# Optimization experiments

Hardware: AMD Instinct MI355X
Metric: run time of the kernel (lower is better)

Reference implementation:

```python
import jax, jax.numpy as jnp
import numpy as np

LEAK = 0.01
TEMP = 1.0
N_ORB = 1024
CTX = 32
N_ALPHA = 32
N_BETA = 32
B = 8192
EPS = 1e-20


def _leaky(x):
    return jnp.where(x >= 0, x, LEAK * x)


def _scorer_mlp(x, W1, b1, W2, b2, W3, b3):
    h = _leaky(x @ W1 + b1)
    h = _leaky(h @ W2 + b2)
    return h @ W3 + b3


def _gumbel_topk(logits, gumbel, k, temp):
    # successive-softmax subset relaxation (Plackett-Luce style)
    scores0 = logits + gumbel

    def step(carry, _):
        scores, khot = carry
        onehot = jax.nn.softmax(scores / temp, axis=-1)
        khot = khot + onehot
        scores = scores + jnp.log(jnp.maximum(1.0 - onehot, EPS))
        return (scores, khot), None

    (_, khot), _ = jax.lax.scan(step, (scores0, jnp.zeros_like(scores0)), None, length=k)
    return khot


def _soft_to_hard(soft, k):
    # straight-through: hard forward, soft backward
    idx = jax.lax.top_k(soft, k)[1]                      # (B, k)
    bidx = jnp.arange(soft.shape[0])[:, None]
    hard = jnp.zeros_like(soft).at[bidx, idx].set(1.0)
    return jax.lax.stop_gradient(hard - soft) + soft


def _lin_init(key, fan_in, fan_out):
    s = 1.0 / np.sqrt(fan_in)
    k1, k2 = jax.random.split(key)
    W = jax.random.uniform(k1, (fan_in, fan_out), minval=-s, maxval=s, dtype=jnp.float32)
    b = jax.random.uniform(k2, (fan_out,), minval=-s, maxval=s, dtype=jnp.float32)
    return W, b


def setup_inputs() -> dict:
    key = jax.random.key(0)
    ks = jax.random.split(key, 12)
    # alpha scorer: input = n_orb (baseline only, context_dim=0)
    W1a, b1a = _lin_init(ks[0], N_ORB, 128)
    W2a, b2a = _lin_init(ks[1], 128, 64)
    W3a, b3a = _lin_init(ks[2], 64, N_ORB)
    # beta scorer: context proj n_orb -> 32, input = n_orb + 32
    Wc, bc = _lin_init(ks[3], N_ORB, CTX)
    W1b, b1b = _lin_init(ks[4], N_ORB + CTX, 128)
    W2b, b2b = _lin_init(ks[5], 128, 64)
    W3b, b3b = _lin_init(ks[6], 64, N_ORB)
    baseline_a = jnp.zeros((N_ORB,), jnp.float32)
    baseline_b = jnp.zeros((N_ORB,), jnp.float32)
    # Gumbel noise: -log(-log(U))
    ua = jax.random.uniform(ks[7], (B, N_ORB), minval=1e-6, maxval=1.0 - 1e-6)
    ub = jax.random.uniform(ks[8], (B, N_ORB), minval=1e-6, maxval=1.0 - 1e-6)
    g_alpha = -jnp.log(-jnp.log(ua))
    g_beta = -jnp.log(-jnp.log(ub))
    return {
        "baseline_a": baseline_a, "W1a": W1a, "b1a": b1a, "W2a": W2a, "b2a": b2a,
        "W3a": W3a, "b3a": b3a,
        "baseline_b": baseline_b, "Wc": Wc, "bc": bc, "W1b": W1b, "b1b": b1b,
        "W2b": W2b, "b2b": b2b, "W3b": W3b, "b3b": b3b,
        "g_alpha": g_alpha, "g_beta": g_beta,
        "batch_size": B,
    }


def reference(baseline_a, W1a, b1a, W2a, b2a, W3a, b3a,
              baseline_b, Wc, bc, W1b, b1b, W2b, b2b, W3b, b3b,
              g_alpha, g_beta, batch_size):
    # --- alpha scoring (context_dim = 0) ---
    base_a = jnp.broadcast_to(baseline_a, (batch_size, N_ORB))
    alpha_logits = _scorer_mlp(base_a, W1a, b1a, W2a, b2a, W3a, b3a) + base_a
    alpha_soft = _gumbel_topk(alpha_logits, g_alpha, N_ALPHA, TEMP)
    alpha_config = _soft_to_hard(alpha_soft, N_ALPHA)          # (B, N_ORB)
    # --- beta scoring conditioned on alpha config ---
    base_b = jnp.broadcast_to(baseline_b, (batch_size, N_ORB))
    ctx = alpha_config @ Wc + bc                               # (B, 32)
    net_in = jnp.concatenate([base_b, ctx], axis=-1)
    beta_logits = _scorer_mlp(net_in, W1b, b1b, W2b, b2b, W3b, b3b) + base_b
    beta_soft = _gumbel_topk(beta_logits, g_beta, N_BETA, TEMP)
    beta_config = _soft_to_hard(beta_soft, N_BETA)
    return jnp.concatenate([alpha_config, beta_config], axis=-1)  # (B, num_sites)
```

## Files before the change

kernel.cpp:

```cpp
#include <hip/hip_runtime.h>
#include <hip/hip_bf16.h>
#include <float.h>

#define N_ORB 1024
#define KSEL 32
#define LEAK 0.01f
#define LOG2E 1.4426950408889634f

typedef float f32x2 __attribute__((ext_vector_type(2)));

__device__ __forceinline__ float leaky(float x) { return x >= 0.0f ? x : LEAK * x; }

__device__ __forceinline__ f32x2 pk_add(f32x2 a, f32x2 b) {
  f32x2 d;
  asm("v_pk_add_f32 %0, %1, %2" : "=v"(d) : "v"(a), "v"(b));
  return d;
}
__device__ __forceinline__ f32x2 pk_mul(f32x2 a, f32x2 b) {
  f32x2 d;
  asm("v_pk_mul_f32 %0, %1, %2" : "=v"(d) : "v"(a), "v"(b));
  return d;
}
__device__ __forceinline__ f32x2 pk_fma(f32x2 a, f32x2 b, f32x2 c) {
  f32x2 d;
  asm("v_pk_fma_f32 %0, %1, %2, %3" : "=v"(d) : "v"(a), "v"(b), "v"(c));
  return d;
}
__device__ __forceinline__ f32x2 pk_fma_clamp(f32x2 a, f32x2 b, f32x2 c) {
  f32x2 d;
  asm("v_pk_fma_f32 %0, %1, %2, %3 clamp" : "=v"(d) : "v"(a), "v"(b), "v"(c));
  return d;
}

template <int CTRL, int RM>
__device__ __forceinline__ int dpp0_i(int v) {
  return __builtin_amdgcn_update_dpp(0, v, CTRL, RM, 0xF, true);
}
template <int CTRL>
__device__ __forceinline__ float dpp_zero(float v) {
  return __int_as_float(
      __builtin_amdgcn_update_dpp(0, __float_as_int(v), CTRL, 0xF, 0xF, true));
}
__device__ __forceinline__ float rdlane(float v, int l) {
  return __int_as_float(__builtin_amdgcn_readlane(__float_as_int(v), l));
}

__device__ __forceinline__ float wave_sum64_dpp(float v) {
  v += dpp_zero<0x111>(v);
  v += dpp_zero<0x112>(v);
  v += dpp_zero<0x114>(v);
  v += dpp_zero<0x118>(v);
  v += dpp_zero<0x142>(v);
  v += dpp_zero<0x143>(v);
  return rdlane(v, 63);
}
__device__ __forceinline__ int wave_isum64(int v) {
  v += dpp0_i<0x111, 0xF>(v);
  v += dpp0_i<0x112, 0xF>(v);
  v += dpp0_i<0x114, 0xF>(v);
  v += dpp0_i<0x118, 0xF>(v);
  v += dpp0_i<0x142, 0xF>(v);
  v += dpp0_i<0x143, 0xF>(v);
  return __builtin_amdgcn_readlane(v, 63);
}
__device__ __forceinline__ int wave_iscan64(int v) {
  v += dpp0_i<0x111, 0xF>(v);
  v += dpp0_i<0x112, 0xF>(v);
  v += dpp0_i<0x114, 0xF>(v);
  v += dpp0_i<0x118, 0xF>(v);
  v += dpp0_i<0x142, 0xA>(v);
  v += dpp0_i<0x143, 0xC>(v);
  return v;
}

__device__ void run_chain2(f32x2 w[16], f32x2 kh[16]) {
#pragma unroll
  for (int i = 0; i < 16; ++i) kh[i] = f32x2{0.0f, 0.0f};
  const f32x2 onev = f32x2{1.0f, 1.0f};
  for (int it = 0; it < KSEL; ++it) {
    f32x2 t0 = pk_add(w[0], w[1]), t1 = pk_add(w[2], w[3]);
    f32x2 t2 = pk_add(w[4], w[5]), t3 = pk_add(w[6], w[7]);
    f32x2 t4 = pk_add(w[8], w[9]), t5 = pk_add(w[10], w[11]);
    f32x2 t6 = pk_add(w[12], w[13]), t7 = pk_add(w[14], w[15]);
    t0 = pk_add(t0, t1); t2 = pk_add(t2, t3);
    t4 = pk_add(t4, t5); t6 = pk_add(t6, t7);
    t0 = pk_add(t0, t2); t4 = pk_add(t4, t6);
    t0 = pk_add(t0, t4);
    float Z0 = wave_sum64_dpp(t0.x);
    float Z1 = wave_sum64_dpp(t0.y);
    Z0 = fmaxf(Z0, 1e-30f);
    Z1 = fmaxf(Z1, 1e-30f);
    float r0 = __builtin_amdgcn_rcpf(Z0);
    float r1 = __builtin_amdgcn_rcpf(Z1);
    float rZ0 = __builtin_fmaf(__builtin_fmaf(-Z0, r0, 1.0f), r0, r0);
    float rZ1 = __builtin_fmaf(__builtin_fmaf(-Z1, r1, 1.0f), r1, r1);
    const f32x2 rZ = f32x2{rZ0, rZ1};
    const f32x2 rZn = f32x2{-rZ0, -rZ1};
#pragma unroll
    for (int i = 0; i < 16; ++i) {
      kh[i] = pk_fma(w[i], rZ, kh[i]);
      f32x2 om = pk_fma_clamp(w[i], rZn, onev);
      w[i] = pk_mul(w[i], om);
    }
  }
}

__device__ unsigned tie_mask16(const f32x2 kh[16], bool comp_y, unsigned T,
                               int lane) {
  unsigned gt = 0, eq = 0;
#pragma unroll
  for (int i = 0; i < 16; ++i) {
    const unsigned u = __float_as_uint(comp_y ? kh[i].y : kh[i].x);
    gt |= (u > T ? 1u : 0u) << i;
    eq |= (u == T ? 1u : 0u) << i;
  }
  const int n_gt = wave_isum64(__popc(gt));
  const int m = 32 - n_gt;
  const int pe = __popc(eq);
  const int be = wave_iscan64(pe) - pe;
  int need = m - be;
  need = need < 0 ? 0 : (need > pe ? pe : need);
  unsigned tk = 0;
  unsigned em = eq;
  for (int guard = 0; guard < 16; ++guard) {
    if (!__any(need > 0)) break;
    if (need > 0) {
      const int bpos = __ffs(em) - 1;
      tk |= 1u << bpos;
      em &= em - 1;
      --need;
    }
  }
  return gt | tk;
}

__device__ void top32_mask2(const f32x2 kh[16], int lane, unsigned& m0,
                            unsigned& m1) {
  unsigned lo0 = 0, lo1 = 0;
  bool ex0 = false, ex1 = false;
  for (int b = 30; b >= 0; --b) {
    const unsigned c0v = lo0 | (1u << b);
    const unsigned c1v = lo1 | (1u << b);
    int c0 = 0, c1 = 0;
#pragma unroll
    for (int i = 0; i < 16; ++i) {
      c0 += __popcll(__ballot(__float_as_uint(kh[i].x) >= c0v));
      c1 += __popcll(__ballot(__float_as_uint(kh[i].y) >= c1v));
    }
    if (!ex0 && c0 >= 32) { lo0 = c0v; ex0 = (c0 == 32); }
    if (!ex1 && c1 >= 32) { lo1 = c1v; ex1 = (c1 == 32); }
    if (ex0 && ex1) break;
  }

  if (ex0) {
    unsigned mk = 0;
#pragma unroll
    for (int i = 0; i < 16; ++i)
      mk |= (__float_as_uint(kh[i].x) >= lo0 ? 1u : 0u) << i;
    m0 = mk;
  } else {
    m0 = tie_mask16(kh, false, lo0, lane);
  }
  if (ex1) {
    unsigned mk = 0;
#pragma unroll
    for (int i = 0; i < 16; ++i)
      mk |= (__float_as_uint(kh[i].y) >= lo1 ? 1u : 0u) << i;
    m1 = mk;
  } else {
    m1 = tie_mask16(kh, true, lo1, lane);
  }
}

__device__ __forceinline__ void compact_idx(unsigned mask, int lane,
                                            int* __restrict__ dst) {
  const int pe = __popc(mask);
  int base = wave_iscan64(pe) - pe;
  unsigned m = mask;
  while (m) {
    const int s = __ffs(m) - 1;
    m &= m - 1;
    dst[base++] = (lane << 4) | s;
  }
}

__device__ __forceinline__ void write_half(float* __restrict__ dst,
                                           unsigned mask, int lane) {
  float4* o4 = (float4*)dst;
#pragma unroll
  for (int q = 0; q < 4; ++q) {
    float4 o;
    o.x = ((mask >> (4 * q + 0)) & 1) ? 1.0f : 0.0f;
    o.y = ((mask >> (4 * q + 1)) & 1) ? 1.0f : 0.0f;
    o.z = ((mask >> (4 * q + 2)) & 1) ? 1.0f : 0.0f;
    o.w = ((mask >> (4 * q + 3)) & 1) ? 1.0f : 0.0f;
    o4[lane * 4 + q] = o;
  }
}


extern "C" __global__ void pcfs_pre1(const float* __restrict__ ba,
                                     const float* __restrict__ W1a,
                                     const float* __restrict__ b1a,
                                     const float* __restrict__ bb,
                                     const float* __restrict__ W1b,
                                     float* __restrict__ ws) {
  const int b = blockIdx.x;
  const int t = threadIdx.x;
  float acc = 0.0f;
  if (b < 128) {
#pragma unroll
    for (int j = t; j < N_ORB; j += 256) acc += ba[j] * W1a[j * 128 + b];
  } else {
    const int n = b - 128;
#pragma unroll
    for (int j = t; j < N_ORB; j += 256) acc += bb[j] * W1b[j * 128 + n];
  }
  __shared__ float red[4];
  float wsum = wave_sum64_dpp(acc);
  if ((t & 63) == 0) red[t >> 6] = wsum;
  __syncthreads();
  if (t == 0) {
    float tot = red[0] + red[1] + red[2] + red[3];
    if (b < 128)
      ws[1152 + b] = leaky(tot + b1a[b]);
    else
      ws[N_ORB + (b - 128)] = tot;
  }
}

extern "C" __global__ void pcfs_pre2a(const float* __restrict__ W2a,
                                      const float* __restrict__ b2a,
                                      float* __restrict__ ws) {
  const int t = threadIdx.x;
  float acc = b2a[t];
#pragma unroll 8
  for (int n = 0; n < 128; ++n) acc = __builtin_fmaf(ws[1152 + n], W2a[n * 64 + t], acc);
  ws[1280 + t] = leaky(acc);
}

extern "C" __global__ void pcfs_pre2b(const float* __restrict__ ba,
                                      const float* __restrict__ W3a,
                                      const float* __restrict__ b3a,
                                      float* __restrict__ ws) {
  __shared__ float h2s[64];
  const int t = threadIdx.x;
  const int o = blockIdx.x * 256 + t;
  if (t < 64) h2s[t] = ws[1280 + t];
  __syncthreads();
  float acc = b3a[o] + ba[o];
#pragma unroll 8
  for (int m = 0; m < 64; ++m) acc = __builtin_fmaf(h2s[m], W3a[m * N_ORB + o], acc);
  ws[o] = acc;
}

extern "C" __global__ void __launch_bounds__(256, 4) pcfs_sampler(
    const float* __restrict__ ws, const float* __restrict__ Wc,
    const float* __restrict__ bc, const float* __restrict__ W1b,
    const float* __restrict__ b1b, const float* __restrict__ W2b,
    const float* __restrict__ b2b, const float* __restrict__ W3b,
    const float* __restrict__ b3b, const float* __restrict__ bb,
    const float* __restrict__ g_alpha, const float* __restrict__ g_beta,
    float* __restrict__ out, int B) {
  __shared__ int sidx[4][64];
  const int wave = threadIdx.x >> 6;
  const int lane = threadIdx.x & 63;
  const int pair = blockIdx.x * 4 + wave;
  const int row0 = pair * 2;
  if (row0 >= B) return;
  const bool have1 = (row0 + 1 < B);
  const int row1 = have1 ? row0 + 1 : row0;

  {
    const int sid = wave + ((blockIdx.x & 3) << 2);
    for (int k = 0; k < sid; ++k) __builtin_amdgcn_s_sleep(1);
  }

  float4 gb0[4], gb1[4];
  {
    const float4* g40 = (const float4*)(g_beta + (size_t)row0 * N_ORB);
    const float4* g41 = (const float4*)(g_beta + (size_t)row1 * N_ORB);
#pragma unroll
    for (int q = 0; q < 4; ++q) {
      gb0[q] = g40[lane * 4 + q];
      gb1[q] = g41[lane * 4 + q];
    }
  }

  f32x2 w[16], kh[16];

  {
    const float4* c4 = (const float4*)ws;
    const float4* g40 = (const float4*)(g_alpha + (size_t)row0 * N_ORB);
    const float4* g41 = (const float4*)(g_alpha + (size_t)row1 * N_ORB);
#pragma unroll
    for (int q = 0; q < 4; ++q) {
      float4 c = c4[lane * 4 + q];
      float4 g0 = g40[lane * 4 + q];
      float4 g1 = g41[lane * 4 + q];
      w[4 * q + 0] = f32x2{__builtin_amdgcn_exp2f((c.x + g0.x) * LOG2E),
                           __builtin_amdgcn_exp2f((c.x + g1.x) * LOG2E)};
      w[4 * q + 1] = f32x2{__builtin_amdgcn_exp2f((c.y + g0.y) * LOG2E),
                           __builtin_amdgcn_exp2f((c.y + g1.y) * LOG2E)};
      w[4 * q + 2] = f32x2{__builtin_amdgcn_exp2f((c.z + g0.z) * LOG2E),
                           __builtin_amdgcn_exp2f((c.z + g1.z) * LOG2E)};
      w[4 * q + 3] = f32x2{__builtin_amdgcn_exp2f((c.w + g0.w) * LOG2E),
                           __builtin_amdgcn_exp2f((c.w + g1.w) * LOG2E)};
    }
  }
  run_chain2(w, kh);
  unsigned am0, am1;
  top32_mask2(kh, lane, am0, am1);

  write_half(out + (size_t)row0 * (2 * N_ORB), am0, lane);
  if (have1) write_half(out + (size_t)row1 * (2 * N_ORB), am1, lane);

  compact_idx(am0, lane, &sidx[wave][0]);
  compact_idx(am1, lane, &sidx[wave][32]);
  const int vi0 = sidx[wave][lane & 31];
  const int vi1 = sidx[wave][32 + (lane & 31)];
  const float bcv = bc[lane & 31];
  float ctx0 = bcv, ctx1 = bcv;
#pragma unroll
  for (int r = 0; r < 32; ++r) {
    const int i0 = __builtin_amdgcn_readlane(vi0, r);
    const int i1 = __builtin_amdgcn_readlane(vi1, r);
    ctx0 += Wc[i0 * 32 + (lane & 31)];
    ctx1 += Wc[i1 * 32 + (lane & 31)];
  }

  f32x2 h1a, h1b_;
  {
    const float ia = b1b[lane] + ws[N_ORB + lane];
    const float ib = b1b[lane + 64] + ws[N_ORB + lane + 64];
    h1a = f32x2{ia, ia};
    h1b_ = f32x2{ib, ib};
  }
#pragma unroll 4
  for (int c = 0; c < 32; ++c) {
    const f32x2 cv = f32x2{rdlane(ctx0, c), rdlane(ctx1, c)};
    const float* wr = W1b + (size_t)(N_ORB + c) * 128;
    const float wa = wr[lane], wb = wr[lane + 64];
    h1a = __builtin_elementwise_fma(f32x2{wa, wa}, cv, h1a);
    h1b_ = __builtin_elementwise_fma(f32x2{wb, wb}, cv, h1b_);
  }
  h1a = f32x2{leaky(h1a.x), leaky(h1a.y)};
  h1b_ = f32x2{leaky(h1b_.x), leaky(h1b_.y)};

  f32x2 h2p0, h2p1, h2p2, h2p3;
  {
    const float i2 = b2b[lane];
    h2p0 = f32x2{i2, i2};
    h2p1 = f32x2{0.0f, 0.0f};
    h2p2 = f32x2{0.0f, 0.0f};
    h2p3 = f32x2{0.0f, 0.0f};
  }
#pragma unroll 4
  for (int n = 0; n < 64; n += 4) {
    const f32x2 v0 = f32x2{rdlane(h1a.x, n + 0), rdlane(h1a.y, n + 0)};
    const f32x2 v1 = f32x2{rdlane(h1a.x, n + 1), rdlane(h1a.y, n + 1)};
    const f32x2 v2 = f32x2{rdlane(h1a.x, n + 2), rdlane(h1a.y, n + 2)};
    const f32x2 v3 = f32x2{rdlane(h1a.x, n + 3), rdlane(h1a.y, n + 3)};
    const float w0 = W2b[(n + 0) * 64 + lane];
    const float w1 = W2b[(n + 1) * 64 + lane];
    const float w2 = W2b[(n + 2) * 64 + lane];
    const float w3 = W2b[(n + 3) * 64 + lane];
    h2p0 = __builtin_elementwise_fma(f32x2{w0, w0}, v0, h2p0);
    h2p1 = __builtin_elementwise_fma(f32x2{w1, w1}, v1, h2p1);
    h2p2 = __builtin_elementwise_fma(f32x2{w2, w2}, v2, h2p2);
    h2p3 = __builtin_elementwise_fma(f32x2{w3, w3}, v3, h2p3);
  }
#pragma unroll 4
  for (int n = 0; n < 64; n += 4) {
    const f32x2 v0 = f32x2{rdlane(h1b_.x, n + 0), rdlane(h1b_.y, n + 0)};
    const f32x2 v1 = f32x2{rdlane(h1b_.x, n + 1), rdlane(h1b_.y, n + 1)};
    const f32x2 v2 = f32x2{rdlane(h1b_.x, n + 2), rdlane(h1b_.y, n + 2)};
    const f32x2 v3 = f32x2{rdlane(h1b_.x, n + 3), rdlane(h1b_.y, n + 3)};
    const float w0 = W2b[(n + 64 + 0) * 64 + lane];
    const float w1 = W2b[(n + 64 + 1) * 64 + lane];
    const float w2 = W2b[(n + 64 + 2) * 64 + lane];
    const float w3 = W2b[(n + 64 + 3) * 64 + lane];
    h2p0 = __builtin_elementwise_fma(f32x2{w0, w0}, v0, h2p0);
    h2p1 = __builtin_elementwise_fma(f32x2{w1, w1}, v1, h2p1);
    h2p2 = __builtin_elementwise_fma(f32x2{w2, w2}, v2, h2p2);
    h2p3 = __builtin_elementwise_fma(f32x2{w3, w3}, v3, h2p3);
  }
  f32x2 h2v = (h2p0 + h2p1) + (h2p2 + h2p3);
  h2v = f32x2{leaky(h2v.x), leaky(h2v.y)};

  {
    const float4* b4 = (const float4*)b3b;
#pragma unroll
    for (int q = 0; q < 4; ++q) {
      float4 b = b4[lane * 4 + q];
      w[4 * q + 0] = f32x2{b.x, b.x};
      w[4 * q + 1] = f32x2{b.y, b.y};
      w[4 * q + 2] = f32x2{b.z, b.z};
      w[4 * q + 3] = f32x2{b.w, b.w};
    }
  }
#pragma unroll 4
  for (int m = 0; m < 64; ++m) {
    const f32x2 hm = f32x2{rdlane(h2v.x, m), rdlane(h2v.y, m)};
    const float4* w4 = (const float4*)(W3b + m * N_ORB);
#pragma unroll
    for (int q = 0; q < 4; ++q) {
      float4 wv = w4[lane * 4 + q];
      w[4 * q + 0] = __builtin_elementwise_fma(f32x2{wv.x, wv.x}, hm, w[4 * q + 0]);
      w[4 * q + 1] = __builtin_elementwise_fma(f32x2{wv.y, wv.y}, hm, w[4 * q + 1]);
      w[4 * q + 2] = __builtin_elementwise_fma(f32x2{wv.z, wv.z}, hm, w[4 * q + 2]);
      w[4 * q + 3] = __builtin_elementwise_fma(f32x2{wv.w, wv.w}, hm, w[4 * q + 3]);
    }
  }
  {
    const float4* bb4 = (const float4*)bb;
#pragma unroll
    for (int q = 0; q < 4; ++q) {
      float4 b = bb4[lane * 4 + q];
      const float4 g0 = gb0[q];
      const float4 g1 = gb1[q];
      w[4 * q + 0] = f32x2{
          __builtin_amdgcn_exp2f((w[4 * q + 0].x + b.x + g0.x) * LOG2E),
          __builtin_amdgcn_exp2f((w[4 * q + 0].y + b.x + g1.x) * LOG2E)};
      w[4 * q + 1] = f32x2{
          __builtin_amdgcn_exp2f((w[4 * q + 1].x + b.y + g0.y) * LOG2E),
          __builtin_amdgcn_exp2f((w[4 * q + 1].y + b.y + g1.y) * LOG2E)};
      w[4 * q + 2] = f32x2{
          __builtin_amdgcn_exp2f((w[4 * q + 2].x + b.z + g0.z) * LOG2E),
          __builtin_amdgcn_exp2f((w[4 * q + 2].y + b.z + g1.z) * LOG2E)};
      w[4 * q + 3] = f32x2{
          __builtin_amdgcn_exp2f((w[4 * q + 3].x + b.w + g0.w) * LOG2E),
          __builtin_amdgcn_exp2f((w[4 * q + 3].y + b.w + g1.w) * LOG2E)};
    }
  }
  run_chain2(w, kh);
  unsigned bm0, bm1;
  top32_mask2(kh, lane, bm0, bm1);

  write_half(out + (size_t)row0 * (2 * N_ORB) + N_ORB, bm0, lane);
  if (have1) write_half(out + (size_t)row1 * (2 * N_ORB) + N_ORB, bm1, lane);
}

extern "C" void kernel_launch(void* const* d_in, const int* in_sizes, int n_in,
                              void* d_out, int out_size, void* d_ws, size_t ws_size,
                              hipStream_t stream) {
  const float* ba  = (const float*)d_in[0];
  const float* W1a = (const float*)d_in[1];
  const float* b1a = (const float*)d_in[2];
  const float* W2a = (const float*)d_in[3];
  const float* b2a = (const float*)d_in[4];
  const float* W3a = (const float*)d_in[5];
  const float* b3a = (const float*)d_in[6];
  const float* bb  = (const float*)d_in[7];
  const float* Wc  = (const float*)d_in[8];
  const float* bc  = (const float*)d_in[9];
  const float* W1b = (const float*)d_in[10];
  const float* b1b = (const float*)d_in[11];
  const float* W2b = (const float*)d_in[12];
  const float* b2b = (const float*)d_in[13];
  const float* W3b = (const float*)d_in[14];
  const float* b3b = (const float*)d_in[15];
  const float* ga  = (const float*)d_in[16];
  const float* gbt = (const float*)d_in[17];
  const int B = in_sizes[16] / N_ORB;
  float* ws = (float*)d_ws;

  hipLaunchKernelGGL(pcfs_pre1, dim3(256), dim3(256), 0, stream,
                     ba, W1a, b1a, bb, W1b, ws);
  hipLaunchKernelGGL(pcfs_pre2a, dim3(1), dim3(64), 0, stream,
                     W2a, b2a, ws);
  hipLaunchKernelGGL(pcfs_pre2b, dim3(4), dim3(256), 0, stream,
                     ba, W3a, b3a, ws);
  const int pairs = (B + 1) / 2;
  hipLaunchKernelGGL(pcfs_sampler, dim3((pairs + 3) / 4), dim3(256), 0, stream,
                     ws, Wc, bc, W1b, b1b, W2b, b2b, W3b, b3b, bb,
                     ga, gbt, (float*)d_out, B);
}
```

Baseline: 278.3 us.

## Stage W3b tiles in shared memory shared by all four waves

The beta-scorer output layer now loads W3b in 8-row tiles (32 KB) into LDS cooperatively with block-wide barriers, and all four waves read from LDS instead of each streaming W3b from global/L2. To make the barriers safe, early return for out-of-range waves is replaced with predicated writes, and the staggered s_sleep startup is removed. The added LDS (32 KB per block) may cut occupancy under the 4-block launch bound, and the 16 barriers couple the waves' progress.

```diff
diff --git a/kernel.cpp b/kernel.cpp
--- a/kernel.cpp
+++ b/kernel.cpp
@@ -263,23 +263,21 @@
     const float* __restrict__ g_alpha, const float* __restrict__ g_beta,
     float* __restrict__ out, int B) {
   __shared__ int sidx[4][64];
-  const int wave = threadIdx.x >> 6;
-  const int lane = threadIdx.x & 63;
+  __shared__ float w3s[8 * N_ORB];
+  const int tid = threadIdx.x;
+  const int wave = tid >> 6;
+  const int lane = tid & 63;
   const int pair = blockIdx.x * 4 + wave;
   const int row0 = pair * 2;
-  if (row0 >= B) return;
-  const bool have1 = (row0 + 1 < B);
-  const int row1 = have1 ? row0 + 1 : row0;
-
-  {
-    const int sid = wave + ((blockIdx.x & 3) << 2);
-    for (int k = 0; k < sid; ++k) __builtin_amdgcn_s_sleep(1);
-  }
+  const bool active = (row0 < B);
+  const bool have1 = active && (row0 + 1 < B);
+  const int r0 = active ? row0 : 0;
+  const int r1 = have1 ? row0 + 1 : r0;
 
   float4 gb0[4], gb1[4];
   {
-    const float4* g40 = (const float4*)(g_beta + (size_t)row0 * N_ORB);
-    const float4* g41 = (const float4*)(g_beta + (size_t)row1 * N_ORB);
+    const float4* g40 = (const float4*)(g_beta + (size_t)r0 * N_ORB);
+    const float4* g41 = (const float4*)(g_beta + (size_t)r1 * N_ORB);
 #pragma unroll
     for (int q = 0; q < 4; ++q) {
       gb0[q] = g40[lane * 4 + q];
@@ -291,8 +289,8 @@
 
   {
     const float4* c4 = (const float4*)ws;
-    const float4* g40 = (const float4*)(g_alpha + (size_t)row0 * N_ORB);
-    const float4* g41 = (const float4*)(g_alpha + (size_t)row1 * N_ORB);
+    const float4* g40 = (const float4*)(g_alpha + (size_t)r0 * N_ORB);
+    const float4* g41 = (const float4*)(g_alpha + (size_t)r1 * N_ORB);
 #pragma unroll
     for (int q = 0; q < 4; ++q) {
       float4 c = c4[lane * 4 + q];
@@ -312,8 +310,8 @@
   unsigned am0, am1;
   top32_mask2(kh, lane, am0, am1);
 
-  write_half(out + (size_t)row0 * (2 * N_ORB), am0, lane);
-  if (have1) write_half(out + (size_t)row1 * (2 * N_ORB), am1, lane);
+  if (active) write_half(out + (size_t)row0 * (2 * N_ORB), am0, lane);
+  if (have1) write_half(out + (size_t)(row0 + 1) * (2 * N_ORB), am1, lane);
 
   compact_idx(am0, lane, &sidx[wave][0]);
   compact_idx(am1, lane, &sidx[wave][32]);
@@ -399,17 +397,28 @@
       w[4 * q + 3] = f32x2{b.w, b.w};
     }
   }
-#pragma unroll 4
-  for (int m = 0; m < 64; ++m) {
-    const f32x2 hm = f32x2{rdlane(h2v.x, m), rdlane(h2v.y, m)};
-    const float4* w4 = (const float4*)(W3b + m * N_ORB);
-#pragma unroll
-    for (int q = 0; q < 4; ++q) {
-      float4 wv = w4[lane * 4 + q];
-      w[4 * q + 0] = __builtin_elementwise_fma(f32x2{wv.x, wv.x}, hm, w[4 * q + 0]);
-      w[4 * q + 1] = __builtin_elementwise_fma(f32x2{wv.y, wv.y}, hm, w[4 * q + 1]);
-      w[4 * q + 2] = __builtin_elementwise_fma(f32x2{wv.z, wv.z}, hm, w[4 * q + 2]);
-      w[4 * q + 3] = __builtin_elementwise_fma(f32x2{wv.w, wv.w}, hm, w[4 * q + 3]);
+  for (int t = 0; t < 8; ++t) {
+    __syncthreads();
+    {
+      const float4* src = (const float4*)(W3b + (size_t)t * 8 * N_ORB);
+      float4* dst = (float4*)w3s;
+#pragma unroll
+      for (int k = 0; k < 8; ++k) dst[tid + k * 256] = src[tid + k * 256];
+    }
+    __syncthreads();
+#pragma unroll
+    for (int ml = 0; ml < 8; ++ml) {
+      const int m = t * 8 + ml;
+      const f32x2 hm = f32x2{rdlane(h2v.x, m), rdlane(h2v.y, m)};
+      const float4* w4 = (const float4*)(w3s + ml * N_ORB);
+#pragma unroll
+      for (int q = 0; q < 4; ++q) {
+        float4 wv = w4[lane * 4 + q];
+        w[4 * q + 0] = __builtin_elementwise_fma(f32x2{wv.x, wv.x}, hm, w[4 * q + 0]);
+        w[4 * q + 1] = __builtin_elementwise_fma(f32x2{wv.y, wv.y}, hm, w[4 * q + 1]);
+        w[4 * q + 2] = __builtin_elementwise_fma(f32x2{wv.z, wv.z}, hm, w[4 * q + 2]);
+        w[4 * q + 3] = __builtin_elementwise_fma(f32x2{wv.w, wv.w}, hm, w[4 * q + 3]);
+      }
     }
   }
   {
@@ -437,8 +446,9 @@
   unsigned bm0, bm1;
   top32_mask2(kh, lane, bm0, bm1);
 
-  write_half(out + (size_t)row0 * (2 * N_ORB) + N_ORB, bm0, lane);
-  if (have1) write_half(out + (size_t)row1 * (2 * N_ORB) + N_ORB, bm1, lane);
+  if (active) write_half(out + (size_t)row0 * (2 * N_ORB) + N_ORB, bm0, lane);
+  if (have1)
+    write_half(out + (size_t)(row0 + 1) * (2 * N_ORB) + N_ORB, bm1, lane);
 }
 
 extern "C" void kernel_launch(void* const* d_in, const int* in_sizes, int n_in,
```

New measurement: 268.8 us. 3.4% less time.
